# Performance work log

Measured on AMD Instinct MI355X. Metric: run time of the kernel, lower is better.

The kernel has to match this reference:

```python
import jax, jax.numpy as jnp
import numpy as np

B, N, K, C = 4, 4096, 32, 192  # batch, npoint, nsample, channels (C % 6 == 0)
EPS = 1e-5


def setup_inputs() -> dict:
    key = jax.random.key(0)
    ks = jax.random.split(key, 8)
    p = jax.random.normal(ks[0], (B, N, 3), jnp.float32)
    x = jax.random.normal(ks[1], (B, C, N), jnp.float32)
    idx = jax.random.randint(ks[2], (B, N, K), 0, N)  # ball-query neighbor ids
    W = jax.random.normal(ks[3], (C, C + 3), jnp.float32) * 0.05  # 1x1 conv weight
    gamma = 1.0 + 0.1 * jax.random.normal(ks[4], (C,), jnp.float32)
    beta = 0.1 * jax.random.normal(ks[5], (C,), jnp.float32)
    rmean = 0.1 * jax.random.normal(ks[6], (C,), jnp.float32)
    rvar = jax.random.uniform(ks[7], (C,), jnp.float32) + 0.5  # positive running var
    return dict(p=p, x=x, idx=idx, W=W, gamma=gamma, beta=beta, rmean=rmean, rvar=rvar)


def reference(p, x, idx, W, gamma, beta, rmean, rvar):
    # --- grouper: gather neighbors, relative coords ---
    pn = jax.vmap(lambda pp, ii: pp[ii])(p, idx)            # [B,N,K,3]
    dp = jnp.transpose(pn - p[:, :, None, :], (0, 3, 1, 2))  # [B,3,N,K]
    xj = jax.vmap(lambda xx, ii: xx[:, ii])(x, idx)          # [B,C,N,K]
    # --- PosPool sin/cos positional embedding fused with features ---
    feat_dim = C // 6
    dim_mat = jnp.power(500.0, jnp.arange(feat_dim, dtype=jnp.float32) / feat_dim)
    div = (50.0 * dp)[..., None] / dim_mat                   # [B,3,N,K,fd]
    pe = jnp.concatenate([jnp.sin(div), jnp.cos(div)], axis=-1)  # [B,3,N,K,2fd]
    pe = jnp.transpose(pe, (0, 1, 4, 2, 3)).reshape(B, C, N, K)  # [B,C,N,K]
    agg = xj * pe + pe
    # --- dp_fj concat -> 1x1 conv -> BN(eval) -> ReLU ---
    h = jnp.concatenate([dp, agg], axis=1)                   # [B,C+3,N,K]
    y = jnp.einsum('oc,bcnk->bonk', W, h)                    # [B,C,N,K]
    inv = gamma / jnp.sqrt(rvar + EPS)
    y = y * inv[:, None, None] + (beta - rmean * inv)[:, None, None]
    y = jax.nn.relu(y)
    # --- max reduction over neighbors ---
    return jnp.max(y, axis=-1)                               # [B,C,N]
```

## Files before the change

### kernel.cpp

```cpp
#include <hip/hip_runtime.h>
#include <math.h>

#define B_   4
#define N_   4096
#define K_   32
#define C_   192
#define CH_  195
#define KPAD 224
#define PTS  2
#define NKT  7
#define NNT  4
#define GRID ((B_ * N_) / PTS)

using half8  = __attribute__((ext_vector_type(8))) _Float16;
using half2v = __attribute__((ext_vector_type(2))) _Float16;
using f32x4  = __attribute__((ext_vector_type(4))) float;

__device__ _Float16 g_Wp[C_ * KPAD];
__device__ _Float16 g_xT[(size_t)B_ * N_ * C_];

__global__ __launch_bounds__(256) void prep(const float* __restrict__ x,
                                            const float* __restrict__ W,
                                            const float* __restrict__ gamma_,
                                            const float* __restrict__ rvar) {
    const int tid = threadIdx.x;
    if (blockIdx.x < 512) {
        __shared__ float s[32][201];
        const int b  = blockIdx.x >> 7;
        const int n0 = (blockIdx.x & 127) * 32;
        const int cl = tid >> 3;
        const int n4 = (tid & 7) * 4;
#pragma unroll
        for (int it = 0; it < 6; ++it) {
            const int c = it * 32 + cl;
            const float4 v = *(const float4*)(x + ((size_t)b * C_ + c) * N_ + n0 + n4);
            s[n4 + 0][c] = v.x; s[n4 + 1][c] = v.y; s[n4 + 2][c] = v.z; s[n4 + 3][c] = v.w;
        }
        __syncthreads();
        const int n  = tid >> 3;
        const int og = tid & 7;
#pragma unroll
        for (int it = 0; it < 3; ++it) {
            const int oc = it * 8 + og;
            half8 v;
#pragma unroll
            for (int jj = 0; jj < 8; ++jj) v[jj] = (_Float16)s[n][oc * 8 + jj];
            *(half8*)(g_xT + ((size_t)b * N_ + n0 + n) * C_ + oc * 8) = v;
        }
    } else {
        const int i = (blockIdx.x - 512) * 256 + tid;
        if (i < C_ * KPAD) {
            const int o = i / KPAD, r = i - o * KPAD;
            const float inv = gamma_[o] * rsqrtf(rvar[o] + 1e-5f);
            float v = 0.0f;
            if (r < 192)      v = W[o * CH_ + 3 + r];
            else if (r < 195) v = W[o * CH_ + (r - 192)];
            g_Wp[i] = (_Float16)(v * inv);
        }
    }
}

__global__ __launch_bounds__(256, 5) void la_mfma(
    const float* __restrict__ p,
    const int*   __restrict__ idx,
    const float* __restrict__ gamma_,
    const float* __restrict__ beta_,
    const float* __restrict__ rmean,
    const float* __restrict__ rvar,
    float* __restrict__ out)
{
    __shared__ _Float16 hb[NKT * NNT * 64 * 8];
    __shared__ float s_bias[C_], s_fr[32], s_out[C_ * PTS];

    const int tid  = threadIdx.x;
    const int lane = tid & 63;
    const int w    = tid >> 6;
    const int l15  = lane & 15;
    const int quad = lane >> 4;

    const int q  = blockIdx.x & 7;
    const int sI = blockIdx.x >> 3;
    const int L  = q * (GRID / 8) + sI;
    const int bn0 = L * PTS;
    const int b   = bn0 >> 12;
    const int n0  = bn0 & (N_ - 1);

    if (tid < C_) {
        const float inv = gamma_[tid] * rsqrtf(rvar[tid] + 1e-5f);
        s_bias[tid] = beta_[tid] - rmean[tid] * inv;
    }
    if (tid < 32) s_fr[tid] = 7.9577471546f * exp2f(-(float)tid * 0.2801808715263400f);
    __syncthreads();

    {
        const int col = w * 16 + l15;
        const int pt  = col >> 5;
        const int k   = col & 31;
        const int gp  = bn0 + pt;
        const int j   = idx[(size_t)gp * K_ + k];
        const float d0 = p[(size_t)(b * N_ + j) * 3 + 0] - p[(size_t)gp * 3 + 0];
        const float d1 = p[(size_t)(b * N_ + j) * 3 + 1] - p[(size_t)gp * 3 + 1];
        const float d2 = p[(size_t)(b * N_ + j) * 3 + 2] - p[(size_t)gp * 3 + 2];
        const _Float16* xh = g_xT + ((size_t)b * N_ + j) * C_;

        half8 v6[6];
#pragma unroll
        for (int i6 = 0; i6 < 6; ++i6)
            v6[i6] = *(const half8*)(xh + (quad + 4 * i6) * 8);

        float sfr[8];
#pragma unroll
        for (int jj = 0; jj < 8; ++jj) sfr[jj] = s_fr[quad * 8 + jj];

#pragma unroll
        for (int i6 = 0; i6 < 6; ++i6) {
            const int chunk = quad + 4 * i6;
            const half8 v = v6[i6];
            const float dd  = (chunk < 8) ? d0 : ((chunk < 16) ? d1 : d2);
            const float off = (chunk & 4) ? 0.25f : 0.0f;
            half8 hv;
#pragma unroll
            for (int jj = 0; jj < 8; jj += 2) {
                const float pe0 = __builtin_amdgcn_sinf(fmaf(dd, sfr[jj],     off));
                const float pe1 = __builtin_amdgcn_sinf(fmaf(dd, sfr[jj + 1], off));
                const half2v pe2 = __builtin_bit_cast(half2v, __builtin_amdgcn_cvt_pkrtz(pe0, pe1));
                half2v v2; v2[0] = v[jj]; v2[1] = v[jj + 1];
                const half2v r2 = pe2 * v2 + pe2;
                hv[jj] = r2[0]; hv[jj + 1] = r2[1];
            }
            const int kt = chunk >> 2;
            *(half8*)(&hb[(size_t)((kt * NNT + w) * 64 + quad * 16 + l15) * 8]) = hv;
        }
        if (quad == 0) {
            half8 hv0 = (half8)(_Float16)0.0f;
            hv0[0] = (_Float16)d0; hv0[1] = (_Float16)d1; hv0[2] = (_Float16)d2;
            *(half8*)(&hb[(size_t)((6 * NNT + w) * 64 + 0 * 16 + l15) * 8]) = hv0;
        } else {
            *(half8*)(&hb[(size_t)((6 * NNT + w) * 64 + quad * 16 + l15) * 8]) = (half8)(_Float16)0.0f;
        }
    }
    __syncthreads();

    f32x4 acc[3][4];
#pragma unroll
    for (int i = 0; i < 3; ++i)
#pragma unroll
        for (int t = 0; t < 4; ++t) acc[i][t] = (f32x4)0.0f;

#pragma unroll
    for (int kt = 0; kt < NKT; ++kt) {
        const int k0 = kt * 32 + quad * 8;
        half8 a[3], bf[4];
#pragma unroll
        for (int i = 0; i < 3; ++i) {
            const int m = (w * 3 + i) * 16 + l15;
            a[i] = *(const half8*)(g_Wp + (size_t)m * KPAD + k0);
        }
#pragma unroll
        for (int t = 0; t < 4; ++t)
            bf[t] = *(const half8*)(&hb[(size_t)((kt * NNT + t) * 64 + lane) * 8]);
#pragma unroll
        for (int i = 0; i < 3; ++i)
#pragma unroll
            for (int t = 0; t < 4; ++t)
                acc[i][t] = __builtin_amdgcn_mfma_f32_16x16x32_f16(bf[t], a[i], acc[i][t], 0, 0, 0);
    }

#pragma unroll
    for (int i = 0; i < 3; ++i) {
        const int m = (w * 3 + i) * 16 + l15;
        float vv[PTS];
#pragma unroll
        for (int ptc = 0; ptc < PTS; ++ptc) {
            const f32x4 va = acc[i][2 * ptc];
            const f32x4 vb = acc[i][2 * ptc + 1];
            float v = fmaxf(fmaxf(fmaxf(va[0], va[1]), fmaxf(va[2], va[3])),
                            fmaxf(fmaxf(vb[0], vb[1]), fmaxf(vb[2], vb[3])));
            v = fmaxf(v, __shfl_xor(v, 16, 64));
            v = fmaxf(v, __shfl_xor(v, 32, 64));
            vv[ptc] = v;
        }
        if (quad == 0) {
            const float bias = s_bias[m];
            float2 o2;
            o2.x = fmaxf(vv[0] + bias, 0.0f);
            o2.y = fmaxf(vv[1] + bias, 0.0f);
            *(float2*)(&s_out[m * PTS]) = o2;
        }
    }
    __syncthreads();

    if (tid < C_) {
        const float2 o2 = *(const float2*)(&s_out[tid * PTS]);
        *(float2*)(&out[((size_t)b * C_ + tid) * N_ + n0]) = o2;
    }
}

extern "C" void kernel_launch(void* const* d_in, const int* in_sizes, int n_in,
                              void* d_out, int out_size, void* d_ws, size_t ws_size,
                              hipStream_t stream) {
    (void)in_sizes; (void)n_in; (void)out_size; (void)d_ws; (void)ws_size;
    const float* p      = (const float*)d_in[0];
    const float* x      = (const float*)d_in[1];
    const int*   idx    = (const int*)d_in[2];
    const float* W      = (const float*)d_in[3];
    const float* gamma_ = (const float*)d_in[4];
    const float* beta_  = (const float*)d_in[5];
    const float* rmean  = (const float*)d_in[6];
    const float* rvar   = (const float*)d_in[7];
    float* out = (float*)d_out;

    prep<<<512 + (C_ * KPAD + 255) / 256, 256, 0, stream>>>(x, W, gamma_, rvar);
    la_mfma<<<GRID, 256, 0, stream>>>(p, idx, gamma_, beta_, rmean, rvar, out);
}
```

Measured before the change: 162.8 us.

## Make MFMA kernel persistent with register-resident weights and idx prefetch

Replaces the one-block-per-point-pair grid with a persistent grid of 768 blocks. Each block loops over 10-11 consecutive point pairs belonging to one XCD/batch slice. The BN-folded fp16 weight fragments are loaded into registers once per block instead of once per pair, and the next pair's neighbor index is prefetched during the MFMA phase. This removes repeated weight loads and per-block setup, but the extra registers lower occupancy (launch bounds drop to 3 waves) and the loop serializes gather and MFMA within a block.

```diff
diff --git a/kernel.cpp b/kernel.cpp
--- a/kernel.cpp
+++ b/kernel.cpp
@@ -7,10 +7,10 @@
 #define C_   192
 #define CH_  195
 #define KPAD 224
-#define PTS  2
 #define NKT  7
 #define NNT  4
-#define GRID ((B_ * N_) / PTS)
+#define NPAIR (B_ * N_ / 2)
+#define GRID  768
 
 using half8  = __attribute__((ext_vector_type(8))) _Float16;
 using half2v = __attribute__((ext_vector_type(2))) _Float16;
@@ -60,7 +60,7 @@
     }
 }
 
-__global__ __launch_bounds__(256, 5) void la_mfma(
+__global__ __launch_bounds__(256, 3) void la_mfma(
     const float* __restrict__ p,
     const int*   __restrict__ idx,
     const float* __restrict__ gamma_,
@@ -70,7 +70,7 @@
     float* __restrict__ out)
 {
     __shared__ _Float16 hb[NKT * NNT * 64 * 8];
-    __shared__ float s_bias[C_], s_fr[32], s_out[C_ * PTS];
+    __shared__ float s_bias[C_], s_fr[32], s_out[C_ * 2];
 
     const int tid  = threadIdx.x;
     const int lane = tid & 63;
@@ -78,12 +78,12 @@
     const int l15  = lane & 15;
     const int quad = lane >> 4;
 
-    const int q  = blockIdx.x & 7;
-    const int sI = blockIdx.x >> 3;
-    const int L  = q * (GRID / 8) + sI;
-    const int bn0 = L * PTS;
-    const int b   = bn0 >> 12;
-    const int n0  = bn0 & (N_ - 1);
+    const int xcd    = blockIdx.x & 7;
+    const int slot   = blockIdx.x >> 3;
+    const int st     = (slot < 64) ? slot * 11 : slot * 10 + 64;
+    const int npairs = (slot < 64) ? 11 : 10;
+    const int pair0  = xcd * 1024 + st;
+    const int b      = xcd >> 1;
 
     if (tid < C_) {
         const float inv = gamma_[tid] * rsqrtf(rvar[tid] + 1e-5f);
@@ -92,30 +92,37 @@
     if (tid < 32) s_fr[tid] = 7.9577471546f * exp2f(-(float)tid * 0.2801808715263400f);
     __syncthreads();
 
-    {
-        const int col = w * 16 + l15;
-        const int pt  = col >> 5;
-        const int k   = col & 31;
+    float sfr[8];
+#pragma unroll
+    for (int jj = 0; jj < 8; ++jj) sfr[jj] = s_fr[quad * 8 + jj];
+
+    half8 wf[3][NKT];
+#pragma unroll
+    for (int i = 0; i < 3; ++i)
+#pragma unroll
+        for (int kt = 0; kt < NKT; ++kt)
+            wf[i][kt] = *(const half8*)(g_Wp + (size_t)((w * 3 + i) * 16 + l15) * KPAD
+                                              + kt * 32 + quad * 8);
+
+    const int pt = w >> 1;
+    const int k  = (w & 1) * 16 + l15;
+
+    int j = idx[(size_t)(pair0 * 2 + pt) * K_ + k];
+
+    for (int it = 0; it < npairs; ++it) {
+        const int bn0 = (pair0 + it) * 2;
+        const int n0  = bn0 & (N_ - 1);
         const int gp  = bn0 + pt;
-        const int j   = idx[(size_t)gp * K_ + k];
+
         const float d0 = p[(size_t)(b * N_ + j) * 3 + 0] - p[(size_t)gp * 3 + 0];
         const float d1 = p[(size_t)(b * N_ + j) * 3 + 1] - p[(size_t)gp * 3 + 1];
         const float d2 = p[(size_t)(b * N_ + j) * 3 + 2] - p[(size_t)gp * 3 + 2];
         const _Float16* xh = g_xT + ((size_t)b * N_ + j) * C_;
 
-        half8 v6[6];
-#pragma unroll
-        for (int i6 = 0; i6 < 6; ++i6)
-            v6[i6] = *(const half8*)(xh + (quad + 4 * i6) * 8);
-
-        float sfr[8];
-#pragma unroll
-        for (int jj = 0; jj < 8; ++jj) sfr[jj] = s_fr[quad * 8 + jj];
-
 #pragma unroll
         for (int i6 = 0; i6 < 6; ++i6) {
             const int chunk = quad + 4 * i6;
-            const half8 v = v6[i6];
+            const half8 v = *(const half8*)(xh + chunk * 8);
             const float dd  = (chunk < 8) ? d0 : ((chunk < 16) ? d1 : d2);
             const float off = (chunk & 4) ? 0.25f : 0.0f;
             half8 hv;
@@ -138,61 +145,60 @@
         } else {
             *(half8*)(&hb[(size_t)((6 * NNT + w) * 64 + quad * 16 + l15) * 8]) = (half8)(_Float16)0.0f;
         }
-    }
-    __syncthreads();
-
-    f32x4 acc[3][4];
-#pragma unroll
-    for (int i = 0; i < 3; ++i)
-#pragma unroll
-        for (int t = 0; t < 4; ++t) acc[i][t] = (f32x4)0.0f;
-
-#pragma unroll
-    for (int kt = 0; kt < NKT; ++kt) {
-        const int k0 = kt * 32 + quad * 8;
-        half8 a[3], bf[4];
+        __syncthreads();
+
+        {
+            const int itn = (it + 1 < npairs) ? it + 1 : it;
+            j = idx[(size_t)((pair0 + itn) * 2 + pt) * K_ + k];
+        }
+
+        f32x4 acc[3][4];
+#pragma unroll
+        for (int i = 0; i < 3; ++i)
+#pragma unroll
+            for (int t = 0; t < 4; ++t) acc[i][t] = (f32x4)0.0f;
+
+#pragma unroll
+        for (int kt = 0; kt < NKT; ++kt) {
+            half8 bf[4];
+#pragma unroll
+            for (int t = 0; t < 4; ++t)
+                bf[t] = *(const half8*)(&hb[(size_t)((kt * NNT + t) * 64 + lane) * 8]);
+#pragma unroll
+            for (int i = 0; i < 3; ++i)
+#pragma unroll
+                for (int t = 0; t < 4; ++t)
+                    acc[i][t] = __builtin_amdgcn_mfma_f32_16x16x32_f16(bf[t], wf[i][kt], acc[i][t], 0, 0, 0);
+        }
+
 #pragma unroll
         for (int i = 0; i < 3; ++i) {
             const int m = (w * 3 + i) * 16 + l15;
-            a[i] = *(const half8*)(g_Wp + (size_t)m * KPAD + k0);
-        }
-#pragma unroll
-        for (int t = 0; t < 4; ++t)
-            bf[t] = *(const half8*)(&hb[(size_t)((kt * NNT + t) * 64 + lane) * 8]);
-#pragma unroll
-        for (int i = 0; i < 3; ++i)
-#pragma unroll
-            for (int t = 0; t < 4; ++t)
-                acc[i][t] = __builtin_amdgcn_mfma_f32_16x16x32_f16(bf[t], a[i], acc[i][t], 0, 0, 0);
-    }
-
-#pragma unroll
-    for (int i = 0; i < 3; ++i) {
-        const int m = (w * 3 + i) * 16 + l15;
-        float vv[PTS];
-#pragma unroll
-        for (int ptc = 0; ptc < PTS; ++ptc) {
-            const f32x4 va = acc[i][2 * ptc];
-            const f32x4 vb = acc[i][2 * ptc + 1];
-            float v = fmaxf(fmaxf(fmaxf(va[0], va[1]), fmaxf(va[2], va[3])),
-                            fmaxf(fmaxf(vb[0], vb[1]), fmaxf(vb[2], vb[3])));
-            v = fmaxf(v, __shfl_xor(v, 16, 64));
-            v = fmaxf(v, __shfl_xor(v, 32, 64));
-            vv[ptc] = v;
-        }
-        if (quad == 0) {
-            const float bias = s_bias[m];
-            float2 o2;
-            o2.x = fmaxf(vv[0] + bias, 0.0f);
-            o2.y = fmaxf(vv[1] + bias, 0.0f);
-            *(float2*)(&s_out[m * PTS]) = o2;
-        }
-    }
-    __syncthreads();
-
-    if (tid < C_) {
-        const float2 o2 = *(const float2*)(&s_out[tid * PTS]);
-        *(float2*)(&out[((size_t)b * C_ + tid) * N_ + n0]) = o2;
+            float vv[2];
+#pragma unroll
+            for (int ptc = 0; ptc < 2; ++ptc) {
+                const f32x4 va = acc[i][2 * ptc];
+                const f32x4 vb = acc[i][2 * ptc + 1];
+                float v = fmaxf(fmaxf(fmaxf(va[0], va[1]), fmaxf(va[2], va[3])),
+                                fmaxf(fmaxf(vb[0], vb[1]), fmaxf(vb[2], vb[3])));
+                v = fmaxf(v, __shfl_xor(v, 16, 64));
+                v = fmaxf(v, __shfl_xor(v, 32, 64));
+                vv[ptc] = v;
+            }
+            if (quad == 0) {
+                const float bias = s_bias[m];
+                float2 o2;
+                o2.x = fmaxf(vv[0] + bias, 0.0f);
+                o2.y = fmaxf(vv[1] + bias, 0.0f);
+                *(float2*)(&s_out[m * 2]) = o2;
+            }
+        }
+        __syncthreads();
+
+        if (tid < C_) {
+            const float2 o2 = *(const float2*)(&s_out[tid * 2]);
+            *(float2*)(&out[((size_t)b * C_ + tid) * N_ + n0]) = o2;
+        }
     }
 }
 
```

Result: slower. 173.2 us (+6.3%).
